# Kernel tuning notes

Hardware: AMD Instinct MI355X
Metric: run time of the kernel (lower is better)

The kernel has to match this reference:

```python
import jax, jax.numpy as jnp
import numpy as np
import math

B, T, C, H = 2, 2048, 1024, 16
D = C // H
EPS = 1e-5

def _layer_norm(x, w, b):
    m = jnp.mean(x, axis=-1, keepdims=True)
    v = jnp.mean((x - m) ** 2, axis=-1, keepdims=True)
    return (x - m) * jax.lax.rsqrt(v + EPS) * w + b

def setup_inputs() -> dict:
    key = jax.random.key(0)
    ks = jax.random.split(key, 8)
    s_attn = 1.0 / math.sqrt(C)
    s_fc = 1.0 / math.sqrt(C)
    s_fc2 = 1.0 / math.sqrt(4 * C)
    return {
        "x": jax.random.normal(ks[0], (B, T, C), dtype=jnp.float32),
        "ln1_w": jnp.ones((C,), jnp.float32),
        "ln1_b": jnp.zeros((C,), jnp.float32),
        "w_qkv": jax.random.normal(ks[1], (C, 3 * C), jnp.float32) * s_attn,  # [in,out]
        "b_qkv": jnp.zeros((3 * C,), jnp.float32),
        "w_proj": jax.random.normal(ks[2], (C, C), jnp.float32) * s_attn,
        "b_proj": jnp.zeros((C,), jnp.float32),
        "ln2_w": jnp.ones((C,), jnp.float32),
        "ln2_b": jnp.zeros((C,), jnp.float32),
        "w_fc": jax.random.normal(ks[3], (C, 4 * C), jnp.float32) * s_fc,
        "b_fc": jnp.zeros((4 * C,), jnp.float32),
        "w_fc2": jax.random.normal(ks[4], (4 * C, C), jnp.float32) * s_fc2,
        "b_fc2": jnp.zeros((C,), jnp.float32),
    }

def reference(x, ln1_w, ln1_b, w_qkv, b_qkv, w_proj, b_proj,
              ln2_w, ln2_b, w_fc, b_fc, w_fc2, b_fc2):
    # --- attention branch ---
    h = _layer_norm(x, ln1_w, ln1_b)
    qkv = h @ w_qkv + b_qkv                      # [B,T,3C]
    q, k, v = jnp.split(qkv, 3, axis=-1)
    # [B,T,C] -> [B,H,T,D]
    q = q.reshape(B, T, H, D).transpose(0, 2, 1, 3)
    k = k.reshape(B, T, H, D).transpose(0, 2, 1, 3)
    v = v.reshape(B, T, H, D).transpose(0, 2, 1, 3)
    scale = 1.0 / math.sqrt(D)
    scores = jnp.einsum("bhtd,bhsd->bhts", q, k) * scale  # [B,H,T,T]
    causal = jnp.tril(jnp.ones((T, T), dtype=bool))
    scores = jnp.where(causal, scores, -jnp.inf)
    attn_w = jax.nn.softmax(scores, axis=-1)     # dropout_p = 0.0
    attn_out = jnp.einsum("bhts,bhsd->bhtd", attn_w, v)
    attn_out = attn_out.transpose(0, 2, 1, 3).reshape(B, T, C)
    attn_out = attn_out @ w_proj + b_proj
    x = x + attn_out
    # --- MLP branch ---
    h2 = _layer_norm(x, ln2_w, ln2_b)
    h2 = jax.nn.gelu(h2 @ w_fc + b_fc, approximate=False)
    x = x + (h2 @ w_fc2 + b_fc2)
    return x, jnp.mean(attn_w, axis=0)           # ([B,T,C], [H,T,T])
```

## Files before the change

### kernel.cpp

```cpp
#include <hip/hip_runtime.h>
#include <cmath>

#define BB 2
#define TT 2048
#define CC 1024
#define HH 16
#define DD 64

typedef unsigned short u16;
typedef __attribute__((ext_vector_type(8))) short bf16x8;
typedef __attribute__((ext_vector_type(8))) _Float16 f16x8;
typedef __attribute__((ext_vector_type(4))) float f32x4;

__device__ __forceinline__ u16 f2bf(float f) {
    union { float f; unsigned u; } v; v.f = f;
    return (u16)((v.u + 0x7fff + ((v.u >> 16) & 1)) >> 16);
}

__device__ __forceinline__ u16 f2h(float f) {
    union { _Float16 h; u16 u; } v; v.h = (_Float16)f;
    return v.u;
}

__device__ __forceinline__ float fexp2(float x) {
    float r; asm("v_exp_f32 %0, %1" : "=v"(r) : "v"(x)); return r;
}

__device__ __forceinline__ float gelu_exact(float v) {
    return 0.5f * v * (1.0f + erff(v * 0.70710678118654752440f));
}

__device__ __forceinline__ void glds16(const void* g, void* l) {
    __builtin_amdgcn_global_load_lds(
        (const __attribute__((address_space(1))) void*)g,
        (__attribute__((address_space(3))) void*)l, 16, 0, 0);
}

__global__ __launch_bounds__(256) void wcvt_kernel(const float* __restrict__ W,
                                                   u16* __restrict__ WT,
                                                   int K, int N) {
    __shared__ u16 t[64][65];
    const int n0 = blockIdx.x * 64, k0 = blockIdx.y * 64;
    const int tid = threadIdx.x;
    const int c = tid & 63;
#pragma unroll
    for (int it = 0; it < 16; ++it) {
        int r = it * 4 + (tid >> 6);
        t[c][r] = f2bf(W[(size_t)(k0 + r) * N + n0 + c]);
    }
    __syncthreads();
#pragma unroll
    for (int it = 0; it < 16; ++it) {
        int r = it * 4 + (tid >> 6);
        WT[(size_t)(n0 + r) * K + k0 + c] = t[r][c];
    }
}

__global__ __launch_bounds__(256) void ln_kernel(const float* __restrict__ x,
                                                 const float* __restrict__ w,
                                                 const float* __restrict__ b,
                                                 u16* __restrict__ out) {
    const int tid = threadIdx.x;
    const int lane = tid & 63;
    const int row = blockIdx.x * 4 + (tid >> 6);
    const float* xr = x + (size_t)row * CC;
    u16* orow = out + (size_t)row * CC;

    float4 v[4];
#pragma unroll
    for (int k = 0; k < 4; ++k)
        v[k] = *reinterpret_cast<const float4*>(xr + k * 256 + lane * 4);

    float s = 0.f;
#pragma unroll
    for (int k = 0; k < 4; ++k) s += v[k].x + v[k].y + v[k].z + v[k].w;
#pragma unroll
    for (int off = 1; off < 64; off <<= 1) s += __shfl_xor(s, off);
    const float mean = s * (1.0f / CC);

    float sq = 0.f;
#pragma unroll
    for (int k = 0; k < 4; ++k) {
        float dx = v[k].x - mean, dy = v[k].y - mean, dz = v[k].z - mean, dw = v[k].w - mean;
        sq += dx * dx + dy * dy + dz * dz + dw * dw;
    }
#pragma unroll
    for (int off = 1; off < 64; off <<= 1) sq += __shfl_xor(sq, off);
    const float rstd = rsqrtf(sq * (1.0f / CC) + 1e-5f);

#pragma unroll
    for (int k = 0; k < 4; ++k) {
        const int c = k * 256 + lane * 4;
        float4 w4 = *reinterpret_cast<const float4*>(w + c);
        float4 b4 = *reinterpret_cast<const float4*>(b + c);
        ushort4 o = make_ushort4(f2bf((v[k].x - mean) * rstd * w4.x + b4.x),
                                 f2bf((v[k].y - mean) * rstd * w4.y + b4.y),
                                 f2bf((v[k].z - mean) * rstd * w4.z + b4.z),
                                 f2bf((v[k].w - mean) * rstd * w4.w + b4.w));
        *reinterpret_cast<ushort4*>(orow + c) = o;
    }
}

template <int EPI, int OUTBF, int WM, int WN, int FI, int FJ>
__global__ __launch_bounds__(256) void gemm_mfma(const u16* __restrict__ A,
                                                 const u16* __restrict__ BT,
                                                 const float* __restrict__ bias,
                                                 const float* __restrict__ res,
                                                 void* __restrict__ out,
                                                 u16* __restrict__ kg,
                                                 u16* __restrict__ vtg,
                                                 int M, int N, int K) {
    constexpr int TM = WM * FI * 16;
    constexpr int TN = WN * FJ * 16;
    __shared__ u16 As[TM * 64];
    __shared__ u16 Bs[TN * 64];

    const int tid = threadIdx.x;
    const int lane = tid & 63;
    const int w = tid >> 6;
    const int wr = w / WN, wc = w % WN;
    const int m16 = lane & 15;
    const int quad = lane >> 4;

    const int bm = blockIdx.y * TM;
    const int bn = blockIdx.x * TN;

    f32x4 acc[FI][FJ] = {};

    for (int k0 = 0; k0 < K; k0 += 64) {
#pragma unroll
        for (int it = 0; it < TM / 32; ++it) {
            int c = w * (TM / 32) + it;
            int q = c * 64 + lane;
            int row = q >> 3;
            int col = ((q & 7) ^ (row & 7)) * 8;
            glds16(&A[(size_t)(bm + row) * K + k0 + col], &As[c * 512]);
        }
#pragma unroll
        for (int it = 0; it < TN / 32; ++it) {
            int c = w * (TN / 32) + it;
            int q = c * 64 + lane;
            int row = q >> 3;
            int col = ((q & 7) ^ (row & 7)) * 8;
            glds16(&BT[(size_t)(bn + row) * K + k0 + col], &Bs[c * 512]);
        }
        __syncthreads();

#pragma unroll
        for (int ks = 0; ks < 2; ++ks) {
            const int co = (ks * 32 + quad * 8) ^ ((m16 & 7) << 3);
            bf16x8 a[FI], b[FJ];
#pragma unroll
            for (int i = 0; i < FI; ++i)
                a[i] = *(const bf16x8*)&As[(wr * FI * 16 + 16 * i + m16) * 64 + co];
#pragma unroll
            for (int j = 0; j < FJ; ++j)
                b[j] = *(const bf16x8*)&Bs[(wc * FJ * 16 + 16 * j + m16) * 64 + co];
#pragma unroll
            for (int i = 0; i < FI; ++i)
#pragma unroll
                for (int j = 0; j < FJ; ++j)
                    acc[i][j] = __builtin_amdgcn_mfma_f32_16x16x32_bf16(a[i], b[j], acc[i][j], 0, 0, 0);
        }
        __syncthreads();
    }

    const int reg3 = bn >> 10;
#pragma unroll
    for (int i = 0; i < FI; ++i) {
        const int row = bm + wr * FI * 16 + 16 * i + quad * 4;
#pragma unroll
        for (int j = 0; j < FJ; ++j) {
            const int col = bn + wc * FJ * 16 + 16 * j + m16;
            const float bv = bias[col];
#pragma unroll
            for (int r = 0; r < 4; ++r) {
                float v = acc[i][j][r] + bv;
                if (EPI == 1) v = gelu_exact(v);
                if (EPI == 2) v += res[(size_t)(row + r) * N + col];
                if (EPI == 3) {
                    if (reg3 == 0) {
                        ((float*)out)[(size_t)(row + r) * N + col] = v;
                    } else {
                        const int rowg = row + r;
                        const int b = rowg >> 11, t = rowg & 2047;
                        const int st = t >> 6, s = t & 63;
                        const int hh = (col >> 6) & 15, d = col & 63;
                        const size_t base = ((size_t)((b * 16 + hh) * 32 + st)) * 4096;
                        if (reg3 == 1) kg[base + s * 64 + (d ^ ((s & 7) << 3))] = f2h(v);
                        else           vtg[base + d * 64 + (s ^ ((d & 7) << 3))] = f2h(v);
                    }
                } else if (OUTBF) {
                    ((u16*)out)[(size_t)(row + r) * N + col] = f2bf(v);
                } else {
                    ((float*)out)[(size_t)(row + r) * N + col] = v;
                }
            }
        }
    }
}

__global__ __launch_bounds__(256) void attn_kernel(const float* __restrict__ qkv,
                                                   const u16* __restrict__ Kg,
                                                   const u16* __restrict__ VTg,
                                                   float* __restrict__ attn_mean,
                                                   u16* __restrict__ attn_out) {
    const int lid = blockIdx.x;
    const int u = lid & 255;
    const int h = u & 15;
    const int ta = u >> 4;
    const int tt = (lid < 256) ? ta : 31 - ta;
    const int t0 = tt * 64;

    const int tid = threadIdx.x;
    const int lane = tid & 63;
    const int w = tid >> 6;
    const int m16 = lane & 15;
    const int quad = lane >> 4;
    const size_t TC3 = 3 * CC;

    __shared__ u16 smem[2][4][4096];
    __shared__ u16 Pm[2][4096];

    const int arow = w * 16 + m16;
    const int sw = (m16 & 7) << 3;
    const int rbase = w * 16 + quad * 4;

    auto toff = [&](int b, int st) -> size_t {
        return ((size_t)((b * 16 + h) * 32 + st)) * 4096;
    };
    auto KSL = [&](int buf, int b) -> const u16 (*)[64] { return (const u16(*)[64]) & smem[buf][b][0]; };
    auto VSL = [&](int buf, int b) -> const u16 (*)[64] { return (const u16(*)[64]) & smem[buf][2 + b][0]; };

    auto stage_tile = [&](const u16* g, u16* l) {
        glds16(g + w * 1024 + lane * 8, l + w * 1024);
        glds16(g + w * 1024 + 512 + lane * 8, l + w * 1024 + 512);
    };
    auto stage_K2 = [&](int buf, int st) {
        stage_tile(Kg + toff(0, st), &smem[buf][0][0]);
        stage_tile(Kg + toff(1, st), &smem[buf][1][0]);
    };
    auto stage_KV4 = [&](int buf, int st) {
        stage_K2(buf, st);
        stage_tile(VTg + toff(0, st), &smem[buf][2][0]);
        stage_tile(VTg + toff(1, st), &smem[buf][3][0]);
    };

    const float QSCALE = 0.125f * 1.4426950408889634f;
    f16x8 qh[2][2];
#pragma unroll
    for (int b = 0; b < 2; ++b) {
        const float* qp = qkv + (size_t)b * TT * TC3 + (size_t)(t0 + arow) * TC3 + h * DD;
#pragma unroll
        for (int ks = 0; ks < 2; ++ks) {
            float4 v0 = *reinterpret_cast<const float4*>(qp + ks * 32 + quad * 8);
            float4 v1 = *reinterpret_cast<const float4*>(qp + ks * 32 + quad * 8 + 4);
            float f[8] = {v0.x, v0.y, v0.z, v0.w, v1.x, v1.y, v1.z, v1.w};
            union { f16x8 v; u16 s[8]; } H;
#pragma unroll
            for (int i = 0; i < 8; ++i) H.s[i] = f2h(f[i] * QSCALE);
            qh[b][ks] = H.v;
        }
    }

    auto compute_S = [&](const f16x8 (&QH)[2], const u16 (*KT)[64],
                         f32x4 (&acc)[4], bool diag) {
        __builtin_amdgcn_s_setprio(1);
#pragma unroll
        for (int ks = 0; ks < 2; ++ks) {
            const int co = (ks * 32 + quad * 8) ^ sw;
#pragma unroll
            for (int j = 0; j < 4; ++j) {
                f16x8 bh = *(const f16x8*)&KT[j * 16 + m16][co];
                acc[j] = __builtin_amdgcn_mfma_f32_16x16x32_f16(QH[ks], bh, acc[j], 0, 0, 0);
            }
        }
        __builtin_amdgcn_s_setprio(0);
        if (diag) {
#pragma unroll
            for (int j = 0; j < 4; ++j)
#pragma unroll
                for (int r = 0; r < 4; ++r)
                    if (j * 16 + m16 > rbase + r) acc[j][r] = -INFINITY;
        }
    };

    auto pv_acc = [&](f32x4 (&O)[4], const u16* Pp, const u16 (*VT)[64]) {
        __builtin_amdgcn_s_setprio(1);
#pragma unroll
        for (int ks = 0; ks < 2; ++ks) {
            const int co = (ks * 32 + quad * 8) ^ sw;
            f16x8 a = *(const f16x8*)&Pp[arow * 64 + co];
#pragma unroll
            for (int j = 0; j < 4; ++j) {
                f16x8 bv = *(const f16x8*)&VT[j * 16 + m16][co];
                O[j] = __builtin_amdgcn_mfma_f32_16x16x32_f16(a, bv, O[j], 0, 0, 0);
            }
        }
        __builtin_amdgcn_s_setprio(0);
    };

    float l_r[2][4] = {};
    stage_K2(0, 0);
    for (int st = 0; st <= tt; ++st) {
        const int cur = st & 1;
        __syncthreads();
        if (st + 1 <= tt) stage_K2(cur ^ 1, st + 1);
        const bool diag = (st == tt);
#pragma unroll
        for (int b = 0; b < 2; ++b) {
            f32x4 acc[4] = {};
            compute_S(qh[b], KSL(cur, b), acc, diag);
#pragma unroll
            for (int r = 0; r < 4; ++r)
                l_r[b][r] += (fexp2(acc[0][r]) + fexp2(acc[1][r])) +
                             (fexp2(acc[2][r]) + fexp2(acc[3][r]));
        }
    }
    __syncthreads();
#pragma unroll
    for (int b = 0; b < 2; ++b)
#pragma unroll
        for (int r = 0; r < 4; ++r) {
            float s = l_r[b][r];
            s += __shfl_xor(s, 1);
            s += __shfl_xor(s, 2);
            s += __shfl_xor(s, 4);
            s += __shfl_xor(s, 8);
            l_r[b][r] = 1.0f / s;
        }

    f32x4 O0[4] = {}, O1[4] = {};
    stage_KV4(0, 0);
    for (int st = 0; st <= tt; ++st) {
        const int cur = st & 1;
        const int s0 = st * 64;
        const bool diag = (st == tt);
        __syncthreads();
        if (st + 1 <= tt) stage_KV4(cur ^ 1, st + 1);

        f32x4 a0[4] = {}, a1[4] = {};
        compute_S(qh[0], KSL(cur, 0), a0, diag);
        compute_S(qh[1], KSL(cur, 1), a1, diag);

#pragma unroll
        for (int j = 0; j < 4; ++j)
#pragma unroll
            for (int r = 0; r < 4; ++r) {
                a0[j][r] = fexp2(a0[j][r]) * l_r[0][r];
                a1[j][r] = fexp2(a1[j][r]) * l_r[1][r];
            }

#pragma unroll
        for (int r = 0; r < 4; ++r) {
            float* mrow = attn_mean + ((size_t)h * TT + t0 + rbase + r) * TT + s0;
#pragma unroll
            for (int j = 0; j < 4; ++j)
                mrow[j * 16 + m16] = 0.5f * (a0[j][r] + a1[j][r]);
        }

#pragma unroll
        for (int r = 0; r < 4; ++r) {
            const int prow = rbase + r;
            const int psw = (prow & 7) << 3;
#pragma unroll
            for (int j = 0; j < 4; ++j) {
                Pm[0][prow * 64 + ((j * 16 + m16) ^ psw)] = f2h(a0[j][r]);
                Pm[1][prow * 64 + ((j * 16 + m16) ^ psw)] = f2h(a1[j][r]);
            }
        }
        pv_acc(O0, &Pm[0][0], VSL(cur, 0));
        pv_acc(O1, &Pm[1][0], VSL(cur, 1));
    }

#pragma unroll
    for (int r = 0; r < 4; ++r) {
        const int trow = t0 + rbase + r;
#pragma unroll
        for (int j = 0; j < 4; ++j) {
            attn_out[((size_t)0 * TT + trow) * CC + h * DD + j * 16 + m16] = f2bf(O0[j][r]);
            attn_out[((size_t)1 * TT + trow) * CC + h * DD + j * 16 + m16] = f2bf(O1[j][r]);
        }
    }

    const int c0 = (tt + 1) * 64;
    const float4 z4 = make_float4(0.f, 0.f, 0.f, 0.f);
    for (int r = 0; r < 64; ++r) {
        float* row = attn_mean + ((size_t)h * TT + t0 + r) * TT;
        for (int c = c0 + tid * 4; c < TT; c += 1024)
            *reinterpret_cast<float4*>(row + c) = z4;
    }
}

extern "C" void kernel_launch(void* const* d_in, const int* in_sizes, int n_in,
                              void* d_out, int out_size, void* d_ws, size_t ws_size,
                              hipStream_t stream) {
    const float* x      = (const float*)d_in[0];
    const float* ln1_w  = (const float*)d_in[1];
    const float* ln1_b  = (const float*)d_in[2];
    const float* w_qkv  = (const float*)d_in[3];
    const float* b_qkv  = (const float*)d_in[4];
    const float* w_proj = (const float*)d_in[5];
    const float* b_proj = (const float*)d_in[6];
    const float* ln2_w  = (const float*)d_in[7];
    const float* ln2_b  = (const float*)d_in[8];
    const float* w_fc   = (const float*)d_in[9];
    const float* b_fc   = (const float*)d_in[10];
    const float* w_fc2  = (const float*)d_in[11];
    const float* b_fc2  = (const float*)d_in[12];

    float* out_x    = (float*)d_out;
    float* out_attn = out_x + (size_t)BB * TT * CC;

    char* wp = (char*)d_ws;
    u16* wT_qkv = (u16*)wp;  wp += (size_t)3072 * 1024 * 2;
    u16* wT_proj = (u16*)wp; wp += (size_t)1024 * 1024 * 2;
    u16* wT_fc  = (u16*)wp;  wp += (size_t)4096 * 1024 * 2;
    u16* wT_fc2 = (u16*)wp;  wp += (size_t)1024 * 4096 * 2;
    u16* h_ln   = (u16*)wp;  wp += (size_t)4096 * 1024 * 2;
    u16* att_o  = (u16*)wp;  wp += (size_t)4096 * 1024 * 2;
    u16* h2     = (u16*)wp;  wp += (size_t)4096 * 4096 * 2;
    float* qkv  = (float*)wp; wp += (size_t)4096 * 3072 * 4;
    float* x1   = (float*)wp; wp += (size_t)4096 * 1024 * 4;

    u16* Kg  = h2;
    u16* VTg = Kg + (size_t)1024 * 4096;

    const int M = BB * TT;

    wcvt_kernel<<<dim3(3072 / 64, 1024 / 64), 256, 0, stream>>>(w_qkv, wT_qkv, 1024, 3072);
    wcvt_kernel<<<dim3(1024 / 64, 1024 / 64), 256, 0, stream>>>(w_proj, wT_proj, 1024, 1024);
    wcvt_kernel<<<dim3(4096 / 64, 1024 / 64), 256, 0, stream>>>(w_fc, wT_fc, 1024, 4096);
    wcvt_kernel<<<dim3(1024 / 64, 4096 / 64), 256, 0, stream>>>(w_fc2, wT_fc2, 4096, 1024);

    ln_kernel<<<M / 4, 256, 0, stream>>>(x, ln1_w, ln1_b, h_ln);
    gemm_mfma<3, 0, 2, 2, 4, 4><<<dim3(3072 / 128, M / 128), 256, 0, stream>>>(
        h_ln, wT_qkv, b_qkv, nullptr, qkv, Kg, VTg, M, 3072, 1024);
    attn_kernel<<<512, 256, 0, stream>>>(qkv, Kg, VTg, out_attn, att_o);
    gemm_mfma<2, 0, 4, 1, 2, 4><<<dim3(1024 / 64, M / 128), 256, 0, stream>>>(
        att_o, wT_proj, b_proj, x, x1, nullptr, nullptr, M, 1024, 1024);
    ln_kernel<<<M / 4, 256, 0, stream>>>(x1, ln2_w, ln2_b, h_ln);
    gemm_mfma<1, 1, 2, 2, 4, 4><<<dim3(4096 / 128, M / 128), 256, 0, stream>>>(
        h_ln, wT_fc, b_fc, nullptr, h2, nullptr, nullptr, M, 4096, 1024);
    gemm_mfma<2, 0, 4, 1, 2, 4><<<dim3(1024 / 64, M / 128), 256, 0, stream>>>(
        h2, wT_fc2, b_fc2, x1, out_x, nullptr, nullptr, M, 1024, 4096);
}
```

Baseline: 654.7 us.

## Double-buffer GEMM LDS, use 512-thread tiles, and restructure K/V layout with transpose kernel

The GEMM now stages the next K-tile into a second LDS buffer while MFMAs run on the current one, and it uses 8 waves per block with larger tiles for all four GEMMs. The QKV epilogue stops scattering K and V into a pre-tiled, swizzled layout and writes plain row-major fp16 K and V plus an fp32 Q buffer. A new transpose kernel builds V^T per head, and attention applies the swizzle while loading into LDS. This aims to hide global-load latency and make the epilogue stores coalesced, at the cost of an extra launch, extra traffic for the V transpose, doubled LDS per block, and fewer blocks for the proj and fc2 GEMMs.

```diff
diff --git a/kernel.cpp b/kernel.cpp
--- a/kernel.cpp
+++ b/kernel.cpp
@@ -102,18 +102,18 @@
 }
 
 template <int EPI, int OUTBF, int WM, int WN, int FI, int FJ>
-__global__ __launch_bounds__(256) void gemm_mfma(const u16* __restrict__ A,
+__global__ __launch_bounds__(512) void gemm_mfma(const u16* __restrict__ A,
                                                  const u16* __restrict__ BT,
                                                  const float* __restrict__ bias,
                                                  const float* __restrict__ res,
                                                  void* __restrict__ out,
-                                                 u16* __restrict__ kg,
-                                                 u16* __restrict__ vtg,
+                                                 u16* __restrict__ kh,
+                                                 u16* __restrict__ vh,
                                                  int M, int N, int K) {
     constexpr int TM = WM * FI * 16;
     constexpr int TN = WN * FJ * 16;
-    __shared__ u16 As[TM * 64];
-    __shared__ u16 Bs[TN * 64];
+    __shared__ u16 As[2][TM * 64];
+    __shared__ u16 Bs[2][TN * 64];
 
     const int tid = threadIdx.x;
     const int lane = tid & 63;
@@ -125,37 +125,43 @@
     const int bm = blockIdx.y * TM;
     const int bn = blockIdx.x * TN;
 
-    f32x4 acc[FI][FJ] = {};
-
-    for (int k0 = 0; k0 < K; k0 += 64) {
-#pragma unroll
-        for (int it = 0; it < TM / 32; ++it) {
-            int c = w * (TM / 32) + it;
+    auto stage = [&](int buf, int kt) {
+        const int k0 = kt * 64;
+#pragma unroll
+        for (int it = 0; it < TM / 64; ++it) {
+            int c = w * (TM / 64) + it;
             int q = c * 64 + lane;
             int row = q >> 3;
             int col = ((q & 7) ^ (row & 7)) * 8;
-            glds16(&A[(size_t)(bm + row) * K + k0 + col], &As[c * 512]);
-        }
-#pragma unroll
-        for (int it = 0; it < TN / 32; ++it) {
-            int c = w * (TN / 32) + it;
+            glds16(&A[(size_t)(bm + row) * K + k0 + col], &As[buf][c * 512]);
+        }
+#pragma unroll
+        for (int it = 0; it < TN / 64; ++it) {
+            int c = w * (TN / 64) + it;
             int q = c * 64 + lane;
             int row = q >> 3;
             int col = ((q & 7) ^ (row & 7)) * 8;
-            glds16(&BT[(size_t)(bn + row) * K + k0 + col], &Bs[c * 512]);
-        }
-        __syncthreads();
-
+            glds16(&BT[(size_t)(bn + row) * K + k0 + col], &Bs[buf][c * 512]);
+        }
+    };
+
+    f32x4 acc[FI][FJ] = {};
+    const int NT = K >> 6;
+    stage(0, 0);
+    __syncthreads();
+    int cur = 0;
+    for (int kt = 0; kt < NT; ++kt) {
+        if (kt + 1 < NT) stage(cur ^ 1, kt + 1);
 #pragma unroll
         for (int ks = 0; ks < 2; ++ks) {
             const int co = (ks * 32 + quad * 8) ^ ((m16 & 7) << 3);
             bf16x8 a[FI], b[FJ];
 #pragma unroll
             for (int i = 0; i < FI; ++i)
-                a[i] = *(const bf16x8*)&As[(wr * FI * 16 + 16 * i + m16) * 64 + co];
+                a[i] = *(const bf16x8*)&As[cur][(wr * FI * 16 + 16 * i + m16) * 64 + co];
 #pragma unroll
             for (int j = 0; j < FJ; ++j)
-                b[j] = *(const bf16x8*)&Bs[(wc * FJ * 16 + 16 * j + m16) * 64 + co];
+                b[j] = *(const bf16x8*)&Bs[cur][(wc * FJ * 16 + 16 * j + m16) * 64 + co];
 #pragma unroll
             for (int i = 0; i < FI; ++i)
 #pragma unroll
@@ -163,9 +169,9 @@
                     acc[i][j] = __builtin_amdgcn_mfma_f32_16x16x32_bf16(a[i], b[j], acc[i][j], 0, 0, 0);
         }
         __syncthreads();
-    }
-
-    const int reg3 = bn >> 10;
+        cur ^= 1;
+    }
+
 #pragma unroll
     for (int i = 0; i < FI; ++i) {
         const int row = bm + wr * FI * 16 + 16 * i + quad * 4;
@@ -179,17 +185,9 @@
                 if (EPI == 1) v = gelu_exact(v);
                 if (EPI == 2) v += res[(size_t)(row + r) * N + col];
                 if (EPI == 3) {
-                    if (reg3 == 0) {
-                        ((float*)out)[(size_t)(row + r) * N + col] = v;
-                    } else {
-                        const int rowg = row + r;
-                        const int b = rowg >> 11, t = rowg & 2047;
-                        const int st = t >> 6, s = t & 63;
-                        const int hh = (col >> 6) & 15, d = col & 63;
-                        const size_t base = ((size_t)((b * 16 + hh) * 32 + st)) * 4096;
-                        if (reg3 == 1) kg[base + s * 64 + (d ^ ((s & 7) << 3))] = f2h(v);
-                        else           vtg[base + d * 64 + (s ^ ((d & 7) << 3))] = f2h(v);
-                    }
+                    if (col < CC) ((float*)out)[(size_t)(row + r) * CC + col] = v;
+                    else if (col < 2 * CC) kh[(size_t)(row + r) * CC + (col - CC)] = f2h(v);
+                    else vh[(size_t)(row + r) * CC + (col - 2 * CC)] = f2h(v);
                 } else if (OUTBF) {
                     ((u16*)out)[(size_t)(row + r) * N + col] = f2bf(v);
                 } else {
@@ -200,9 +198,34 @@
     }
 }
 
-__global__ __launch_bounds__(256) void attn_kernel(const float* __restrict__ qkv,
-                                                   const u16* __restrict__ Kg,
-                                                   const u16* __restrict__ VTg,
+__global__ __launch_bounds__(256) void vtr_kernel(const u16* __restrict__ Vh,
+                                                  u16* __restrict__ VTt) {
+    const int t0 = blockIdx.x * 64;
+    const int h = blockIdx.y;
+    const int b = blockIdx.z;
+    const int tid = threadIdx.x;
+    __shared__ u16 tl[64][65];
+#pragma unroll
+    for (int it = 0; it < 4; ++it) {
+        int e = tid + it * 256;
+        int r = e >> 4, c4 = (e & 15) * 4;
+        ushort4 v = *reinterpret_cast<const ushort4*>(
+            &Vh[(size_t)(b * TT + t0 + r) * CC + h * DD + c4]);
+        tl[c4 + 0][r] = v.x; tl[c4 + 1][r] = v.y; tl[c4 + 2][r] = v.z; tl[c4 + 3][r] = v.w;
+    }
+    __syncthreads();
+#pragma unroll
+    for (int it = 0; it < 4; ++it) {
+        int e = tid + it * 256;
+        int d = e >> 4, s4 = (e & 15) * 4;
+        ushort4 o = make_ushort4(tl[d][s4], tl[d][s4 + 1], tl[d][s4 + 2], tl[d][s4 + 3]);
+        *reinterpret_cast<ushort4*>(&VTt[(size_t)((b * HH + h) * DD + d) * TT + t0 + s4]) = o;
+    }
+}
+
+__global__ __launch_bounds__(256) void attn_kernel(const float* __restrict__ Qf,
+                                                   const u16* __restrict__ Kh,
+                                                   const u16* __restrict__ VTt,
                                                    float* __restrict__ attn_mean,
                                                    u16* __restrict__ attn_out) {
     const int lid = blockIdx.x;
@@ -217,7 +240,6 @@
     const int w = tid >> 6;
     const int m16 = lane & 15;
     const int quad = lane >> 4;
-    const size_t TC3 = 3 * CC;
 
     __shared__ u16 smem[2][4][4096];
     __shared__ u16 Pm[2][4096];
@@ -226,31 +248,39 @@
     const int sw = (m16 & 7) << 3;
     const int rbase = w * 16 + quad * 4;
 
-    auto toff = [&](int b, int st) -> size_t {
-        return ((size_t)((b * 16 + h) * 32 + st)) * 4096;
-    };
     auto KSL = [&](int buf, int b) -> const u16 (*)[64] { return (const u16(*)[64]) & smem[buf][b][0]; };
     auto VSL = [&](int buf, int b) -> const u16 (*)[64] { return (const u16(*)[64]) & smem[buf][2 + b][0]; };
 
-    auto stage_tile = [&](const u16* g, u16* l) {
-        glds16(g + w * 1024 + lane * 8, l + w * 1024);
-        glds16(g + w * 1024 + 512 + lane * 8, l + w * 1024 + 512);
-    };
-    auto stage_K2 = [&](int buf, int st) {
-        stage_tile(Kg + toff(0, st), &smem[buf][0][0]);
-        stage_tile(Kg + toff(1, st), &smem[buf][1][0]);
-    };
+    auto stage_K = [&](int buf, int b, int st) {
+#pragma unroll
+        for (int it = 0; it < 2; ++it) {
+            int c = w * 2 + it;
+            int s = c * 8 + (lane >> 3);
+            int scol = ((lane & 7) * 8) ^ ((s & 7) << 3);
+            glds16(&Kh[(size_t)(b * TT + st * 64 + s) * CC + h * DD + scol],
+                   &smem[buf][b][c * 512]);
+        }
+    };
+    auto stage_V = [&](int buf, int b, int st) {
+#pragma unroll
+        for (int it = 0; it < 2; ++it) {
+            int c = w * 2 + it;
+            int d = c * 8 + (lane >> 3);
+            int scol = ((lane & 7) * 8) ^ ((d & 7) << 3);
+            glds16(&VTt[(size_t)((b * HH + h) * DD + d) * TT + st * 64 + scol],
+                   &smem[buf][2 + b][c * 512]);
+        }
+    };
+    auto stage_K2 = [&](int buf, int st) { stage_K(buf, 0, st); stage_K(buf, 1, st); };
     auto stage_KV4 = [&](int buf, int st) {
-        stage_K2(buf, st);
-        stage_tile(VTg + toff(0, st), &smem[buf][2][0]);
-        stage_tile(VTg + toff(1, st), &smem[buf][3][0]);
+        stage_K2(buf, st); stage_V(buf, 0, st); stage_V(buf, 1, st);
     };
 
     const float QSCALE = 0.125f * 1.4426950408889634f;
     f16x8 qh[2][2];
 #pragma unroll
     for (int b = 0; b < 2; ++b) {
-        const float* qp = qkv + (size_t)b * TT * TC3 + (size_t)(t0 + arow) * TC3 + h * DD;
+        const float* qp = Qf + (size_t)(b * TT + t0 + arow) * CC + h * DD;
 #pragma unroll
         for (int ks = 0; ks < 2; ++ks) {
             float4 v0 = *reinterpret_cast<const float4*>(qp + ks * 32 + quad * 8);
@@ -420,11 +450,12 @@
     u16* h_ln   = (u16*)wp;  wp += (size_t)4096 * 1024 * 2;
     u16* att_o  = (u16*)wp;  wp += (size_t)4096 * 1024 * 2;
     u16* h2     = (u16*)wp;  wp += (size_t)4096 * 4096 * 2;
-    float* qkv  = (float*)wp; wp += (size_t)4096 * 3072 * 4;
+    float* Qf   = (float*)wp; wp += (size_t)4096 * 1024 * 4;
     float* x1   = (float*)wp; wp += (size_t)4096 * 1024 * 4;
 
-    u16* Kg  = h2;
-    u16* VTg = Kg + (size_t)1024 * 4096;
+    u16* Kh  = h2;
+    u16* Vh  = Kh + (size_t)4096 * 1024;
+    u16* VTt = Vh + (size_t)4096 * 1024;
 
     const int M = BB * TT;
 
@@ -434,14 +465,15 @@
     wcvt_kernel<<<dim3(1024 / 64, 4096 / 64), 256, 0, stream>>>(w_fc2, wT_fc2, 4096, 1024);
 
     ln_kernel<<<M / 4, 256, 0, stream>>>(x, ln1_w, ln1_b, h_ln);
-    gemm_mfma<3, 0, 2, 2, 4, 4><<<dim3(3072 / 128, M / 128), 256, 0, stream>>>(
-        h_ln, wT_qkv, b_qkv, nullptr, qkv, Kg, VTg, M, 3072, 1024);
-    attn_kernel<<<512, 256, 0, stream>>>(qkv, Kg, VTg, out_attn, att_o);
-    gemm_mfma<2, 0, 4, 1, 2, 4><<<dim3(1024 / 64, M / 128), 256, 0, stream>>>(
+    gemm_mfma<3, 0, 2, 4, 8, 2><<<dim3(3072 / 128, M / 256), 512, 0, stream>>>(
+        h_ln, wT_qkv, b_qkv, nullptr, Qf, Kh, Vh, M, 3072, 1024);
+    vtr_kernel<<<dim3(TT / 64, HH, BB), 256, 0, stream>>>(Vh, VTt);
+    attn_kernel<<<512, 256, 0, stream>>>(Qf, Kh, VTt, out_attn, att_o);
+    gemm_mfma<2, 0, 2, 4, 4, 2><<<dim3(1024 / 128, M / 128), 512, 0, stream>>>(
         att_o, wT_proj, b_proj, x, x1, nullptr, nullptr, M, 1024, 1024);
     ln_kernel<<<M / 4, 256, 0, stream>>>(x1, ln2_w, ln2_b, h_ln);
-    gemm_mfma<1, 1, 2, 2, 4, 4><<<dim3(4096 / 128, M / 128), 256, 0, stream>>>(
+    gemm_mfma<1, 1, 2, 4, 8, 2><<<dim3(4096 / 128, M / 256), 512, 0, stream>>>(
         h_ln, wT_fc, b_fc, nullptr, h2, nullptr, nullptr, M, 4096, 1024);
-    gemm_mfma<2, 0, 4, 1, 2, 4><<<dim3(1024 / 64, M / 128), 256, 0, stream>>>(
+    gemm_mfma<2, 0, 2, 4, 4, 2><<<dim3(1024 / 128, M / 128), 512, 0, stream>>>(
         h2, wT_fc2, b_fc2, x1, out_x, nullptr, nullptr, M, 1024, 4096);
 }
```

New measurement: 678.5 us. +3.6%, slower.
